# Optimization experiments

Measured on AMD Instinct MI355X. Metric: run time of the kernel, lower is better.

The kernel has to match this reference:

```python
import jax, jax.numpy as jnp
import numpy as np

B, N, F, U, K = 8, 2048, 128, 128, 3
NEG = -1.0e9


def setup_inputs() -> dict:
    key = jax.random.key(0)
    k1, k2, k3, k4, k5 = jax.random.split(key, 5)
    x = jax.random.normal(k1, (B, N, F), dtype=jnp.float32)
    # symmetric binary adjacency, density ~0.005 (avg degree ~20)
    m = (jax.random.uniform(k2, (N, N)) < 0.005).astype(jnp.float32)
    adj = jnp.maximum(m, m.T)
    s_w = np.sqrt(2.0 / (F + U)).astype(np.float32)   # glorot normal
    s_a = np.sqrt(2.0 / (U + N)).astype(np.float32)
    w = jax.random.normal(k3, (K, F, U), dtype=jnp.float32) * s_w
    ai = jax.random.normal(k4, (U, N), dtype=jnp.float32) * s_a
    aj = jax.random.normal(k5, (U, N), dtype=jnp.float32) * s_a
    return {"x": x, "adj": adj, "w": w, "ai": ai, "aj": aj}


def reference(x, adj, w, ai, aj):
    n = adj.shape[0]
    A = adj + jnp.eye(n, dtype=adj.dtype)          # adj + I (self loops)
    A_abs = jnp.abs(A)
    # hop 0
    f = jnp.einsum('bnf,fu->bnu', x, w[0])          # [B,N,U]
    attn = jnp.einsum('bnu,um->bnm', f, ai) \
         + jnp.swapaxes(jnp.einsum('bnu,um->bnm', f, aj), 1, 2)  # [B,N,N]
    attn = attn + NEG * (1.0 - A_abs)
    attn = jax.nn.softmax(attn, axis=1) * A
    a = attn
    # hops 1..k-1
    for i in range(1, w.shape[0]):
        h = jnp.einsum('bnf,bnm->bmf', x, a)        # (x^T @ a)^T, [B,N,F]
        f = jnp.einsum('bmf,fu->bmu', h, w[i]) + f
        a = jnp.matmul(a, attn)
    return jax.nn.relu(f), attn
```

## Files before the change

kernel.cpp:

```cpp
#include <hip/hip_runtime.h>
#include <math.h>

#define B 8
#define N 2048
#define F 128
#define U 128
#define CAP 64


typedef unsigned int uint;
typedef unsigned short ushort;

using short8 = __attribute__((ext_vector_type(8))) short;
using f32x4v = __attribute__((ext_vector_type(4))) float;

__device__ inline ushort f2bf(float v) {
  uint u = __float_as_uint(v);
  u += 0x7fffu + ((u >> 16) & 1u);
  return (ushort)(u >> 16);
}
__device__ inline float bflo(uint p) { return __uint_as_float(p << 16); }
__device__ inline float bfhi(uint p) { return __uint_as_float(p & 0xffff0000u); }

__global__ __launch_bounds__(256) void prep_kernel(
    const float* __restrict__ x, const float* __restrict__ w0,
    const float* __restrict__ ai, const float* __restrict__ aj,
    const float* __restrict__ adj, ushort* __restrict__ f0h,
    ushort* __restrict__ g1h, ushort* __restrict__ g2h,
    float* __restrict__ aiT, ushort* __restrict__ ajTh,
    int* __restrict__ col_idx, int* __restrict__ col_cnt,
    int* __restrict__ col_diag) {
  __shared__ ushort wT[128 * 136];
  const int blk = blockIdx.x;
  const int tid = threadIdx.x;
  if (blk < 512) {
    const int block_row = blk * 32;
    const int wv = tid >> 6, lane = tid & 63;
    const int rt = wv & 1, cg = wv >> 1;
    const int rowbase = block_row + rt * 16;
    const int arow = rowbase + (lane & 15);
    const int asl = (lane >> 4) * 8;
    short8 afr[4];
#pragma unroll
    for (int kk = 0; kk < 4; kk++) {
      const int k0 = kk * 32 + asl;
      float4 xa = *(const float4*)(x + (size_t)arow * F + k0);
      float4 xb = *(const float4*)(x + (size_t)arow * F + k0 + 4);
      afr[kk][0] = (short)f2bf(xa.x); afr[kk][1] = (short)f2bf(xa.y);
      afr[kk][2] = (short)f2bf(xa.z); afr[kk][3] = (short)f2bf(xa.w);
      afr[kk][4] = (short)f2bf(xb.x); afr[kk][5] = (short)f2bf(xb.y);
      afr[kk][6] = (short)f2bf(xb.z); afr[kk][7] = (short)f2bf(xb.w);
    }
    const int crow = rowbase + ((lane >> 4) << 2);
    for (int h = 0; h < 3; h++) {
      __syncthreads();
      for (int idx = tid; idx < 128 * 128; idx += 256) {
        int k = idx >> 7, n = idx & 127;
        wT[n * 136 + k] = f2bf(w0[h * 16384 + idx]);
      }
      __syncthreads();
      f32x4v acc[4];
#pragma unroll
      for (int ct = 0; ct < 4; ct++) acc[ct] = (f32x4v){0.f, 0.f, 0.f, 0.f};
#pragma unroll
      for (int kk = 0; kk < 4; kk++) {
        const int k0 = kk * 32 + asl;
#pragma unroll
        for (int ct = 0; ct < 4; ct++) {
          const int col = cg * 64 + ct * 16 + (lane & 15);
          short8 b = *(const short8*)&wT[col * 136 + k0];
          acc[ct] =
              __builtin_amdgcn_mfma_f32_16x16x32_bf16(afr[kk], b, acc[ct], 0, 0, 0);
        }
      }
      ushort* dst = (h == 0) ? f0h : (h == 1) ? g1h : g2h;
#pragma unroll
      for (int ct = 0; ct < 4; ct++) {
        const int ccol = cg * 64 + ct * 16 + (lane & 15);
#pragma unroll
        for (int r = 0; r < 4; r++)
          dst[(size_t)(crow + r) * U + ccol] = f2bf(acc[ct][r]);
      }
    }
  } else if (blk < 1024) {
    const int m = (blk - 512) * 4 + (tid >> 6);
    const int lane = tid & 63;
    const float* row = adj + (size_t)m * N;
    int cnt = 0;
    int dflag = 0;
    for (int base = 0; base < N; base += 64) {
      int n = base + lane;
      float v = row[n];
      if ((n == m) && (v != 0.f)) dflag = 1;
      bool pred = (v != 0.f) && (n != m);
      unsigned long long mask = __ballot(pred);
      if (pred) {
        int off = cnt + (int)__popcll(mask & ((1ull << lane) - 1ull));
        if (off < CAP - 1) col_idx[m * CAP + off] = n;
      }
      cnt += (int)__popcll(mask);
    }
    unsigned long long dm = __ballot(dflag != 0);
    if (lane == 0) {
      col_cnt[m] = cnt > CAP - 1 ? CAP - 1 : cnt;
      col_diag[m] = dm ? 1 : 0;
    }
  } else {
    int idx = (blk - 1024) * 256 + tid;
    int n = idx >> 7;
    int u = idx & 127;
    aiT[idx] = ai[u * N + n];
    ajTh[idx] = f2bf(aj[u * N + n]);
  }
}

__global__ __launch_bounds__(256) void attn_u_kernel(
    const ushort* __restrict__ f0h, const float* __restrict__ aiT,
    const ushort* __restrict__ ajTh, const ushort* __restrict__ g1h,
    const ushort* __restrict__ g2h, const int* __restrict__ col_idx,
    const int* __restrict__ col_cnt, const int* __restrict__ col_diag,
    float* __restrict__ attn, float* __restrict__ col_val,
    float* __restrict__ dval, ushort* __restrict__ uh) {
  const int wid = (blockIdx.x << 2) + (threadIdx.x >> 6);
  const int lane = threadIdx.x & 63;
  const int b = wid >> 11;
  const int m = wid & 2047;
  const int cnt = col_cnt[m];
  float* attnb = attn + (size_t)b * N * N;
  float* cv = col_val + ((size_t)b * N + m) * CAP;
  const ushort* g2b = g2h + (size_t)b * N * F;
  const size_t oh = ((size_t)b * N + m) * F + 2 * lane;
  const uint g1r = *(const uint*)(g1h + oh);

  if (col_diag[m]) {
    if (lane < cnt) cv[lane] = 0.f;
    if (lane == 0) {
      dval[b * N + m] = 2.f;
      attnb[(size_t)m * N + m] = 2.f;
    }
    uint g2r = *(const uint*)(g2b + m * F + 2 * lane);
    float a0 = bflo(g1r) + 2.f * bflo(g2r);
    float a1 = bfhi(g1r) + 2.f * bfhi(g2r);
    *(uint*)(uh + oh) = (uint)f2bf(a0) | ((uint)f2bf(a1) << 16);
    return;
  }

  const int g = lane >> 4;
  const int s = lane & 15;
  const int nent = cnt + 1;
  const float4 aim0 = *(const float4*)(aiT + m * U + s * 8);
  const float4 aim1 = *(const float4*)(aiT + m * U + s * 8 + 4);
  const uint4 fmv = *(const uint4*)(f0h + ((size_t)b * N + m) * U + s * 8);
  const float fm0 = bflo(fmv.x), fm1 = bfhi(fmv.x);
  const float fm2 = bflo(fmv.y), fm3 = bfhi(fmv.y);
  const float fm4 = bflo(fmv.z), fm5 = bfhi(fmv.z);
  const float fm6 = bflo(fmv.w), fm7 = bfhi(fmv.w);

  float q_own = -INFINITY;
  int n_own = m;
  float mx = -INFINITY;
  int jj = 0;
  for (; (jj + 2) * 4 <= nent; jj += 2) {
    const int e0 = jj * 4 + g;
    const int e1 = e0 + 4;
    int n0 = (e0 == 0) ? m : col_idx[m * CAP + e0 - 1];
    int n1 = col_idx[m * CAP + e1 - 1];
    uint4 fn0 = *(const uint4*)(f0h + ((size_t)b * N + n0) * U + s * 8);
    uint4 an0 = *(const uint4*)(ajTh + n0 * U + s * 8);
    uint4 fn1 = *(const uint4*)(f0h + ((size_t)b * N + n1) * U + s * 8);
    uint4 an1 = *(const uint4*)(ajTh + n1 * U + s * 8);
    float q0 = bflo(fn0.x) * aim0.x + bfhi(fn0.x) * aim0.y +
               bflo(fn0.y) * aim0.z + bfhi(fn0.y) * aim0.w +
               bflo(fn0.z) * aim1.x + bfhi(fn0.z) * aim1.y +
               bflo(fn0.w) * aim1.z + bfhi(fn0.w) * aim1.w +
               fm0 * bflo(an0.x) + fm1 * bfhi(an0.x) + fm2 * bflo(an0.y) +
               fm3 * bfhi(an0.y) + fm4 * bflo(an0.z) + fm5 * bfhi(an0.z) +
               fm6 * bflo(an0.w) + fm7 * bfhi(an0.w);
    float q1 = bflo(fn1.x) * aim0.x + bfhi(fn1.x) * aim0.y +
               bflo(fn1.y) * aim0.z + bfhi(fn1.y) * aim0.w +
               bflo(fn1.z) * aim1.x + bfhi(fn1.z) * aim1.y +
               bflo(fn1.w) * aim1.z + bfhi(fn1.w) * aim1.w +
               fm0 * bflo(an1.x) + fm1 * bfhi(an1.x) + fm2 * bflo(an1.y) +
               fm3 * bfhi(an1.y) + fm4 * bflo(an1.z) + fm5 * bfhi(an1.z) +
               fm6 * bflo(an1.w) + fm7 * bfhi(an1.w);
    q0 += __shfl_xor(q0, 1, 64);
    q1 += __shfl_xor(q1, 1, 64);
    q0 += __shfl_xor(q0, 2, 64);
    q1 += __shfl_xor(q1, 2, 64);
    q0 += __shfl_xor(q0, 4, 64);
    q1 += __shfl_xor(q1, 4, 64);
    q0 += __shfl_xor(q0, 8, 64);
    q1 += __shfl_xor(q1, 8, 64);
    mx = fmaxf(mx, fmaxf(q0, q1));
    if (s == jj) { q_own = q0; n_own = n0; }
    if (s == jj + 1) { q_own = q1; n_own = n1; }
  }
  for (; jj * 4 < nent; jj++) {
    const int e = jj * 4 + g;
    float q = -INFINITY;
    int n = m;
    if (e < nent) {
      n = (e == 0) ? m : col_idx[m * CAP + e - 1];
      uint4 fn = *(const uint4*)(f0h + ((size_t)b * N + n) * U + s * 8);
      uint4 an = *(const uint4*)(ajTh + n * U + s * 8);
      q = bflo(fn.x) * aim0.x + bfhi(fn.x) * aim0.y + bflo(fn.y) * aim0.z +
          bfhi(fn.y) * aim0.w + bflo(fn.z) * aim1.x + bfhi(fn.z) * aim1.y +
          bflo(fn.w) * aim1.z + bfhi(fn.w) * aim1.w + fm0 * bflo(an.x) +
          fm1 * bfhi(an.x) + fm2 * bflo(an.y) + fm3 * bfhi(an.y) +
          fm4 * bflo(an.z) + fm5 * bfhi(an.z) + fm6 * bflo(an.w) +
          fm7 * bfhi(an.w);
    }
    q += __shfl_xor(q, 1, 64);
    q += __shfl_xor(q, 2, 64);
    q += __shfl_xor(q, 4, 64);
    q += __shfl_xor(q, 8, 64);
    mx = fmaxf(mx, q);
    if (s == jj) { q_own = q; n_own = n; }
  }
  mx = fmaxf(mx, __shfl_xor(mx, 16, 64));
  mx = fmaxf(mx, __shfl_xor(mx, 32, 64));
  float e_own = expf(q_own - mx);
  float ssum = e_own;
  ssum += __shfl_xor(ssum, 1, 64);
  ssum += __shfl_xor(ssum, 2, 64);
  ssum += __shfl_xor(ssum, 4, 64);
  ssum += __shfl_xor(ssum, 8, 64);
  ssum += __shfl_xor(ssum, 16, 64);
  ssum += __shfl_xor(ssum, 32, 64);
  const float v_own = e_own / ssum;
  const int eo = s * 4 + g;
  if (eo < nent) {
    if (eo == 0) {
      dval[b * N + m] = v_own;
      attnb[(size_t)m * N + m] = v_own;
    } else {
      cv[eo - 1] = v_own;
      attnb[(size_t)n_own * N + m] = v_own;
    }
  }
  float a0 = bflo(g1r), a1 = bfhi(g1r);
  float b0 = 0.f, b1 = 0.f, c0 = 0.f, c1 = 0.f, d0 = 0.f, d1 = 0.f;
  int e = 0;
  for (; e + 7 < nent; e += 8) {
    int s0 = ((e & 3) << 4) + (e >> 2);
    int s1 = (((e + 1) & 3) << 4) + ((e + 1) >> 2);
    int s2 = (((e + 2) & 3) << 4) + ((e + 2) >> 2);
    int s3 = (((e + 3) & 3) << 4) + ((e + 3) >> 2);
    int s4 = (((e + 4) & 3) << 4) + ((e + 4) >> 2);
    int s5 = (((e + 5) & 3) << 4) + ((e + 5) >> 2);
    int s6 = (((e + 6) & 3) << 4) + ((e + 6) >> 2);
    int s7 = (((e + 7) & 3) << 4) + ((e + 7) >> 2);
    float v0 = __shfl(v_own, s0, 64); int n0 = __shfl(n_own, s0, 64);
    float v1 = __shfl(v_own, s1, 64); int n1 = __shfl(n_own, s1, 64);
    float v2 = __shfl(v_own, s2, 64); int n2 = __shfl(n_own, s2, 64);
    float v3 = __shfl(v_own, s3, 64); int n3 = __shfl(n_own, s3, 64);
    float v4 = __shfl(v_own, s4, 64); int n4 = __shfl(n_own, s4, 64);
    float v5 = __shfl(v_own, s5, 64); int n5 = __shfl(n_own, s5, 64);
    float v6 = __shfl(v_own, s6, 64); int n6 = __shfl(n_own, s6, 64);
    float v7 = __shfl(v_own, s7, 64); int n7 = __shfl(n_own, s7, 64);
    uint gx0 = *(const uint*)(g2b + n0 * F + 2 * lane);
    uint gx1 = *(const uint*)(g2b + n1 * F + 2 * lane);
    uint gx2 = *(const uint*)(g2b + n2 * F + 2 * lane);
    uint gx3 = *(const uint*)(g2b + n3 * F + 2 * lane);
    uint gx4 = *(const uint*)(g2b + n4 * F + 2 * lane);
    uint gx5 = *(const uint*)(g2b + n5 * F + 2 * lane);
    uint gx6 = *(const uint*)(g2b + n6 * F + 2 * lane);
    uint gx7 = *(const uint*)(g2b + n7 * F + 2 * lane);
    a0 += v0 * bflo(gx0); a1 += v0 * bfhi(gx0);
    b0 += v1 * bflo(gx1); b1 += v1 * bfhi(gx1);
    c0 += v2 * bflo(gx2); c1 += v2 * bfhi(gx2);
    d0 += v3 * bflo(gx3); d1 += v3 * bfhi(gx3);
    a0 += v4 * bflo(gx4); a1 += v4 * bfhi(gx4);
    b0 += v5 * bflo(gx5); b1 += v5 * bfhi(gx5);
    c0 += v6 * bflo(gx6); c1 += v6 * bfhi(gx6);
    d0 += v7 * bflo(gx7); d1 += v7 * bfhi(gx7);
  }
  for (; e + 3 < nent; e += 4) {
    int s0 = ((e & 3) << 4) + (e >> 2);
    int s1 = (((e + 1) & 3) << 4) + ((e + 1) >> 2);
    int s2 = (((e + 2) & 3) << 4) + ((e + 2) >> 2);
    int s3 = (((e + 3) & 3) << 4) + ((e + 3) >> 2);
    float v0 = __shfl(v_own, s0, 64); int n0 = __shfl(n_own, s0, 64);
    float v1 = __shfl(v_own, s1, 64); int n1 = __shfl(n_own, s1, 64);
    float v2 = __shfl(v_own, s2, 64); int n2 = __shfl(n_own, s2, 64);
    float v3 = __shfl(v_own, s3, 64); int n3 = __shfl(n_own, s3, 64);
    uint gx0 = *(const uint*)(g2b + n0 * F + 2 * lane);
    uint gx1 = *(const uint*)(g2b + n1 * F + 2 * lane);
    uint gx2 = *(const uint*)(g2b + n2 * F + 2 * lane);
    uint gx3 = *(const uint*)(g2b + n3 * F + 2 * lane);
    a0 += v0 * bflo(gx0); a1 += v0 * bfhi(gx0);
    b0 += v1 * bflo(gx1); b1 += v1 * bfhi(gx1);
    c0 += v2 * bflo(gx2); c1 += v2 * bfhi(gx2);
    d0 += v3 * bflo(gx3); d1 += v3 * bfhi(gx3);
  }
  for (; e < nent; e++) {
    int src = ((e & 3) << 4) + (e >> 2);
    float v = __shfl(v_own, src, 64);
    int n = __shfl(n_own, src, 64);
    uint gx = *(const uint*)(g2b + n * F + 2 * lane);
    a0 += v * bflo(gx);
    a1 += v * bfhi(gx);
  }
  a0 += b0 + c0 + d0;
  a1 += b1 + c1 + d1;
  *(uint*)(uh + oh) = (uint)f2bf(a0) | ((uint)f2bf(a1) << 16);
}

__global__ __launch_bounds__(256) void spmm_out_kernel(
    const ushort* __restrict__ uh, const ushort* __restrict__ f0h,
    const int* __restrict__ col_idx, const int* __restrict__ col_cnt,
    const float* __restrict__ col_val, const float* __restrict__ dval,
    float* __restrict__ out) {
  const int wid = (blockIdx.x << 2) + (threadIdx.x >> 6);
  const int lane = threadIdx.x & 63;
  const int b = wid >> 11;
  const int m = wid & 2047;
  const ushort* inb = uh + (size_t)b * N * F;
  const int cnt = col_cnt[m];
  const float* cv = col_val + ((size_t)b * N + m) * CAP;
  const float dv = dval[b * N + m];
  uint vm = *(const uint*)(inb + m * F + 2 * lane);
  float a0 = dv * bflo(vm);
  float a1 = dv * bfhi(vm);
  float b0 = 0.f, b1 = 0.f, c0 = 0.f, c1 = 0.f, d0 = 0.f, d1 = 0.f;
  int j = 0;
  for (; j + 7 < cnt; j += 8) {
    int n0 = col_idx[m * CAP + j];
    int n1 = col_idx[m * CAP + j + 1];
    int n2 = col_idx[m * CAP + j + 2];
    int n3 = col_idx[m * CAP + j + 3];
    int n4 = col_idx[m * CAP + j + 4];
    int n5 = col_idx[m * CAP + j + 5];
    int n6 = col_idx[m * CAP + j + 6];
    int n7 = col_idx[m * CAP + j + 7];
    float v0 = cv[j], v1 = cv[j + 1], v2 = cv[j + 2], v3 = cv[j + 3];
    float v4 = cv[j + 4], v5 = cv[j + 5], v6 = cv[j + 6], v7 = cv[j + 7];
    uint g0 = *(const uint*)(inb + n0 * F + 2 * lane);
    uint g1 = *(const uint*)(inb + n1 * F + 2 * lane);
    uint g2 = *(const uint*)(inb + n2 * F + 2 * lane);
    uint g3 = *(const uint*)(inb + n3 * F + 2 * lane);
    uint g4 = *(const uint*)(inb + n4 * F + 2 * lane);
    uint g5 = *(const uint*)(inb + n5 * F + 2 * lane);
    uint g6 = *(const uint*)(inb + n6 * F + 2 * lane);
    uint g7 = *(const uint*)(inb + n7 * F + 2 * lane);
    a0 += v0 * bflo(g0); a1 += v0 * bfhi(g0);
    b0 += v1 * bflo(g1); b1 += v1 * bfhi(g1);
    c0 += v2 * bflo(g2); c1 += v2 * bfhi(g2);
    d0 += v3 * bflo(g3); d1 += v3 * bfhi(g3);
    a0 += v4 * bflo(g4); a1 += v4 * bfhi(g4);
    b0 += v5 * bflo(g5); b1 += v5 * bfhi(g5);
    c0 += v6 * bflo(g6); c1 += v6 * bfhi(g6);
    d0 += v7 * bflo(g7); d1 += v7 * bfhi(g7);
  }
  for (; j + 3 < cnt; j += 4) {
    int n0 = col_idx[m * CAP + j];
    int n1 = col_idx[m * CAP + j + 1];
    int n2 = col_idx[m * CAP + j + 2];
    int n3 = col_idx[m * CAP + j + 3];
    float v0 = cv[j], v1 = cv[j + 1], v2 = cv[j + 2], v3 = cv[j + 3];
    uint g0 = *(const uint*)(inb + n0 * F + 2 * lane);
    uint g1 = *(const uint*)(inb + n1 * F + 2 * lane);
    uint g2 = *(const uint*)(inb + n2 * F + 2 * lane);
    uint g3 = *(const uint*)(inb + n3 * F + 2 * lane);
    a0 += v0 * bflo(g0); a1 += v0 * bfhi(g0);
    b0 += v1 * bflo(g1); b1 += v1 * bfhi(g1);
    c0 += v2 * bflo(g2); c1 += v2 * bfhi(g2);
    d0 += v3 * bflo(g3); d1 += v3 * bfhi(g3);
  }
  for (; j < cnt; j++) {
    int n = col_idx[m * CAP + j];
    float v = cv[j];
    uint g = *(const uint*)(inb + n * F + 2 * lane);
    a0 += v * bflo(g);
    a1 += v * bfhi(g);
  }
  a0 += b0 + c0 + d0;
  a1 += b1 + c1 + d1;
  const size_t o = ((size_t)b * N + m) * F + 2 * lane;
  const uint f0r = *(const uint*)(f0h + o);
  float2 ov;
  ov.x = fmaxf(bflo(f0r) + a0, 0.f);
  ov.y = fmaxf(bfhi(f0r) + a1, 0.f);
  *(float2*)(out + o) = ov;
}

extern "C" void kernel_launch(void* const* d_in, const int* in_sizes, int n_in,
                              void* d_out, int out_size, void* d_ws,
                              size_t ws_size, hipStream_t stream) {
  const float* x = (const float*)d_in[0];
  const float* adj = (const float*)d_in[1];
  const float* w = (const float*)d_in[2];
  const float* ai = (const float*)d_in[3];
  const float* aj = (const float*)d_in[4];

  float* out_f = (float*)d_out;
  float* out_attn = out_f + (size_t)B * N * U;

  char* p = (char*)d_ws;
  float* aiT = (float*)p;     p += (size_t)N * U * 4;
  float* col_val = (float*)p; p += (size_t)B * N * CAP * 4;
  float* dval = (float*)p;    p += (size_t)B * N * 4;
  int* col_idx = (int*)p;     p += (size_t)N * CAP * 4;
  int* col_cnt = (int*)p;     p += (size_t)N * 4;
  int* col_diag = (int*)p;    p += (size_t)N * 4;
  ushort* f0h = (ushort*)p;   p += (size_t)B * N * U * 2;
  ushort* ajTh = (ushort*)p;  p += (size_t)N * U * 2;
  ushort* g1h = (ushort*)p;   p += (size_t)B * N * U * 2;
  ushort* g2h = (ushort*)p;   p += (size_t)B * N * U * 2;
  ushort* uh = (ushort*)p;    p += (size_t)B * N * U * 2;

  prep_kernel<<<2048, 256, 0, stream>>>(x, w, ai, aj, adj, f0h, g1h, g2h, aiT,
                                        ajTh, col_idx, col_cnt, col_diag);
  attn_u_kernel<<<B * N / 4, 256, 0, stream>>>(
      f0h, aiT, ajTh, g1h, g2h, col_idx, col_cnt, col_diag, out_attn, col_val,
      dval, uh);
  spmm_out_kernel<<<B * N / 4, 256, 0, stream>>>(uh, f0h, col_idx, col_cnt,
                                                 col_val, dval, out_f);
}
```

Baseline: 67.90 us.

## Share neighbor aj rows across batches via LDS in attention kernel

Blocks of the attention kernel are remapped so that the four waves in a block handle the same node m for four different batches, instead of four different nodes. The block stages the neighbor index list and the gathered bf16 aj rows for m into shared memory once, and all four waves reuse them. This replaces repeated global gathers of the same aj rows and index reads with LDS reads. In exchange it adds two block barriers and a cooperative staging loop, and it gives up the previous spread of nodes across the waves of a block.

```diff
diff --git a/kernel.cpp b/kernel.cpp
--- a/kernel.cpp
+++ b/kernel.cpp
@@ -121,11 +121,15 @@
     const int* __restrict__ col_cnt, const int* __restrict__ col_diag,
     float* __restrict__ attn, float* __restrict__ col_val,
     float* __restrict__ dval, ushort* __restrict__ uh) {
-  const int wid = (blockIdx.x << 2) + (threadIdx.x >> 6);
-  const int lane = threadIdx.x & 63;
-  const int b = wid >> 11;
-  const int m = wid & 2047;
+  __shared__ ushort ajs[64][136];
+  __shared__ int cidx[64];
+  const int m = blockIdx.x >> 1;
+  const int tid = threadIdx.x;
+  const int wv = tid >> 6;
+  const int lane = tid & 63;
+  const int b = ((blockIdx.x & 1) << 2) + wv;
   const int cnt = col_cnt[m];
+  const int nent = cnt + 1;
   float* attnb = attn + (size_t)b * N * N;
   float* cv = col_val + ((size_t)b * N + m) * CAP;
   const ushort* g2b = g2h + (size_t)b * N * F;
@@ -145,9 +149,18 @@
     return;
   }
 
+  if (tid < 64)
+    cidx[tid] = (tid == 0) ? m : ((tid <= cnt) ? col_idx[m * CAP + tid - 1] : m);
+  __syncthreads();
+  for (int i = tid; i < nent * 16; i += 256) {
+    int e = i >> 4, c = i & 15;
+    *(uint4*)&ajs[e][c * 8] =
+        *(const uint4*)(ajTh + (size_t)cidx[e] * U + c * 8);
+  }
+  __syncthreads();
+
   const int g = lane >> 4;
   const int s = lane & 15;
-  const int nent = cnt + 1;
   const float4 aim0 = *(const float4*)(aiT + m * U + s * 8);
   const float4 aim1 = *(const float4*)(aiT + m * U + s * 8 + 4);
   const uint4 fmv = *(const uint4*)(f0h + ((size_t)b * N + m) * U + s * 8);
@@ -163,12 +176,12 @@
   for (; (jj + 2) * 4 <= nent; jj += 2) {
     const int e0 = jj * 4 + g;
     const int e1 = e0 + 4;
-    int n0 = (e0 == 0) ? m : col_idx[m * CAP + e0 - 1];
-    int n1 = col_idx[m * CAP + e1 - 1];
+    int n0 = cidx[e0];
+    int n1 = cidx[e1];
     uint4 fn0 = *(const uint4*)(f0h + ((size_t)b * N + n0) * U + s * 8);
-    uint4 an0 = *(const uint4*)(ajTh + n0 * U + s * 8);
+    uint4 an0 = *(const uint4*)&ajs[e0][s * 8];
     uint4 fn1 = *(const uint4*)(f0h + ((size_t)b * N + n1) * U + s * 8);
-    uint4 an1 = *(const uint4*)(ajTh + n1 * U + s * 8);
+    uint4 an1 = *(const uint4*)&ajs[e1][s * 8];
     float q0 = bflo(fn0.x) * aim0.x + bfhi(fn0.x) * aim0.y +
                bflo(fn0.y) * aim0.z + bfhi(fn0.y) * aim0.w +
                bflo(fn0.z) * aim1.x + bfhi(fn0.z) * aim1.y +
@@ -200,9 +213,9 @@
     float q = -INFINITY;
     int n = m;
     if (e < nent) {
-      n = (e == 0) ? m : col_idx[m * CAP + e - 1];
+      n = cidx[e];
       uint4 fn = *(const uint4*)(f0h + ((size_t)b * N + n) * U + s * 8);
-      uint4 an = *(const uint4*)(ajTh + n * U + s * 8);
+      uint4 an = *(const uint4*)&ajs[e][s * 8];
       q = bflo(fn.x) * aim0.x + bfhi(fn.x) * aim0.y + bflo(fn.y) * aim0.z +
           bfhi(fn.y) * aim0.w + bflo(fn.z) * aim1.x + bfhi(fn.z) * aim1.y +
           bflo(fn.w) * aim1.z + bfhi(fn.w) * aim1.w + fm0 * bflo(an.x) +
@@ -411,9 +424,9 @@
 
   prep_kernel<<<2048, 256, 0, stream>>>(x, w, ai, aj, adj, f0h, g1h, g2h, aiT,
                                         ajTh, col_idx, col_cnt, col_diag);
-  attn_u_kernel<<<B * N / 4, 256, 0, stream>>>(
-      f0h, aiT, ajTh, g1h, g2h, col_idx, col_cnt, col_diag, out_attn, col_val,
-      dval, uh);
+  attn_u_kernel<<<N * 2, 256, 0, stream>>>(f0h, aiT, ajTh, g1h, g2h, col_idx,
+                                           col_cnt, col_diag, out_attn,
+                                           col_val, dval, uh);
   spmm_out_kernel<<<B * N / 4, 256, 0, stream>>>(uh, f0h, col_idx, col_cnt,
                                                  col_val, dval, out_f);
 }
```

Result: no change. 66.86 us, median of 2 (-1.5%).
